# Kernel tuning notes

Measured on AMD Instinct MI355X. Metric: run time of the kernel, lower is better.

Reference implementation:

```python
import jax, jax.numpy as jnp
import numpy as np

B, L, D_MODEL = 2, 4096, 256
EXPAND = 2
D_INNER = EXPAND * D_MODEL
D_STATE = 16
D_CONV = 4
DT_RANK = max(1, D_MODEL // 16)


def setup_inputs() -> dict:
    key = jax.random.key(0)
    ks = jax.random.split(key, 8)
    s = 0.02
    return {
        "x": jax.random.normal(ks[0], (B, L, D_MODEL), jnp.float32),
        "in_proj_w": jax.random.normal(ks[1], (D_MODEL, 2 * D_INNER), jnp.float32) * s,
        "conv_w": jax.random.normal(ks[2], (D_INNER, D_CONV), jnp.float32) * 0.1,
        "conv_b": jnp.zeros((D_INNER,), jnp.float32),
        "x_proj_w": jax.random.normal(ks[3], (D_INNER, DT_RANK + 2 * D_STATE), jnp.float32) * s,
        "dt_proj_w": jax.random.normal(ks[4], (DT_RANK, D_INNER), jnp.float32) * (DT_RANK ** -0.5),
        "dt_proj_b": jnp.log(jnp.expm1(jnp.full((D_INNER,), 0.01, jnp.float32))),
        "A_log": jnp.log(jnp.tile(jnp.arange(1, D_STATE + 1, dtype=jnp.float32), (D_INNER, 1))),
        "D": jnp.ones((D_INNER,), jnp.float32),
        "out_proj_w": jax.random.normal(ks[5], (D_INNER, D_MODEL), jnp.float32) * s,
        "ln_gamma": jnp.ones((D_MODEL,), jnp.float32),
        "ln_beta": jnp.zeros((D_MODEL,), jnp.float32),
    }


def _mamba(x, in_proj_w, conv_w, conv_b, x_proj_w, dt_proj_w, dt_proj_b, A_log, D, out_proj_w):
    b = x.shape[0]
    xz = x @ in_proj_w                       # [B,L,2*d_inner]
    u, z = jnp.split(xz, 2, axis=-1)
    # depthwise causal conv over time
    u_pad = jnp.pad(u, ((0, 0), (D_CONV - 1, 0), (0, 0)))
    kern = conv_w.T[:, None, :]              # [D_CONV, 1, D_INNER]
    u_conv = jax.lax.conv_general_dilated(
        u_pad, kern, (1,), 'VALID',
        dimension_numbers=('NHC', 'HIO', 'NHC'),
        feature_group_count=D_INNER) + conv_b
    u_conv = jax.nn.silu(u_conv)             # [B,L,d_inner]
    dbl = u_conv @ x_proj_w
    dt, Bm, Cm = jnp.split(dbl, [DT_RANK, DT_RANK + D_STATE], axis=-1)
    delta = jax.nn.softplus(dt @ dt_proj_w + dt_proj_b)   # [B,L,d_inner]
    A = -jnp.exp(A_log)                                    # [d_inner,d_state]
    dA = jnp.exp(delta[..., None] * A)                     # [B,L,di,ds]
    dBu = delta[..., None] * Bm[:, :, None, :] * u_conv[..., None]

    def step(h, inputs):
        dA_t, dBu_t, C_t = inputs
        h = dA_t * h + dBu_t                 # [B,di,ds]
        y = jnp.einsum('bdn,bn->bd', h, C_t)
        return h, y

    h0 = jnp.zeros((b, D_INNER, D_STATE), u_conv.dtype)
    _, ys = jax.lax.scan(step, h0,
                         (dA.transpose(1, 0, 2, 3),
                          dBu.transpose(1, 0, 2, 3),
                          Cm.transpose(1, 0, 2)))
    y = ys.transpose(1, 0, 2) + u_conv * D
    y = y * jax.nn.silu(z)
    return y @ out_proj_w


def reference(x, in_proj_w, conv_w, conv_b, x_proj_w, dt_proj_w, dt_proj_b,
              A_log, D, out_proj_w, ln_gamma, ln_beta):
    y = x + _mamba(x, in_proj_w, conv_w, conv_b, x_proj_w, dt_proj_w,
                   dt_proj_b, A_log, D, out_proj_w)
    mu = jnp.mean(y, axis=-1, keepdims=True)
    var = jnp.var(y, axis=-1, keepdims=True)
    return (y - mu) / jnp.sqrt(var + 1e-5) * ln_gamma + ln_beta
```

## Files before the change

kernel.cpp:

```cpp
#include <hip/hip_runtime.h>
#include <math.h>

constexpr int BATCH  = 2;
constexpr int LSEQ   = 4096;
constexpr int DMODEL = 256;
constexpr int DINNER = 512;
constexpr int NST    = 16;
constexpr int MROWS  = BATCH * LSEQ;
constexpr int NCH    = 256;
constexpr int TCH    = LSEQ / NCH;
constexpr float LOG2E = 1.44269504088896f;

typedef __attribute__((ext_vector_type(8))) short bf16x8;
typedef __attribute__((ext_vector_type(4))) float f32x4;

__device__ __forceinline__ float fast_silu(float v) { return v / (1.f + __expf(-v)); }

__device__ __forceinline__ unsigned short f2bf(float f) {
  unsigned int u = __float_as_uint(f);
  u = (u + 0x7fffu + ((u >> 16) & 1u)) >> 16;
  return (unsigned short)u;
}
__device__ __forceinline__ float bf2f(unsigned short u) {
  return __uint_as_float(((unsigned int)u) << 16);
}

__global__ __launch_bounds__(256) void k_cast_x(const float* __restrict__ x,
                                                unsigned short* __restrict__ xb) {
  int i = (blockIdx.x * 256 + threadIdx.x) * 4;
  float4 v = *(const float4*)(x + i);
  ushort4 o;
  o.x = f2bf(v.x); o.y = f2bf(v.y); o.z = f2bf(v.z); o.w = f2bf(v.w);
  *(ushort4*)(xb + i) = o;
}

__global__ __launch_bounds__(256) void k_castT(const float* __restrict__ W,
                                               unsigned short* __restrict__ Wt,
                                               int K, int N, int ktiles) {
  __shared__ float tile[32][33];
  const int bt = blockIdx.x;
  const int kt = bt % ktiles, nt = bt / ktiles;
  const int k0 = kt * 32, n0 = nt * 32;
  const int t = threadIdx.x;
  const int c = t & 31, r0 = t >> 5;
  #pragma unroll
  for (int it = 0; it < 4; ++it) {
    int r = r0 + it * 8;
    tile[r][c] = W[(size_t)(k0 + r) * N + n0 + c];
  }
  __syncthreads();
  #pragma unroll
  for (int it = 0; it < 4; ++it) {
    int cc = r0 + it * 8;
    Wt[(size_t)(n0 + cc) * K + k0 + c] = f2bf(tile[c][cc]);
  }
}

__global__ __launch_bounds__(256) void k_cast_xpw(const float* __restrict__ xpw,
                                                  unsigned short* __restrict__ xpT) {
  int idx = blockIdx.x * 256 + threadIdx.x;
  int n = idx >> 9, k = idx & 511;
  xpT[n * 512 + k] = f2bf(xpw[k * 48 + n]);
}

__global__ __launch_bounds__(256) void k_inproj(const unsigned short* __restrict__ Xb,
                                                const unsigned short* __restrict__ Wt,
                                                unsigned short* __restrict__ ub,
                                                unsigned short* __restrict__ zb) {
  __shared__ unsigned short As[128][40];
  __shared__ unsigned short Bs[128][40];
  const int t = threadIdx.x;
  const int m0 = (blockIdx.x & 63) * 128;
  const int n0 = (blockIdx.x >> 6) * 128;
  const int lane = t & 63, wid = t >> 6;
  const int hi = lane >> 4, l15 = lane & 15;
  const int wm = wid >> 1, wn = wid & 1;
  f32x4 zero = {0.f, 0.f, 0.f, 0.f};
  f32x4 acc[4][4];
  #pragma unroll
  for (int i = 0; i < 4; ++i)
    #pragma unroll
    for (int j = 0; j < 4; ++j) acc[i][j] = zero;

  for (int k0 = 0; k0 < DMODEL; k0 += 32) {
    __syncthreads();
    #pragma unroll
    for (int it = 0; it < 2; ++it) {
      int v = it * 256 + t;
      int r = v >> 2, part = v & 3;
      *(float4*)(&As[r][part * 8]) = *(const float4*)(Xb + (size_t)(m0 + r) * 256 + k0 + part * 8);
      *(float4*)(&Bs[r][part * 8]) = *(const float4*)(Wt + (size_t)(n0 + r) * 256 + k0 + part * 8);
    }
    __syncthreads();
    bf16x8 af[4], bfv[4];
    #pragma unroll
    for (int am = 0; am < 4; ++am) af[am] = *(const bf16x8*)(&As[wm * 64 + am * 16 + l15][hi * 8]);
    #pragma unroll
    for (int bn = 0; bn < 4; ++bn) bfv[bn] = *(const bf16x8*)(&Bs[wn * 64 + bn * 16 + l15][hi * 8]);
    #pragma unroll
    for (int am = 0; am < 4; ++am)
      #pragma unroll
      for (int bn = 0; bn < 4; ++bn)
        acc[am][bn] = __builtin_amdgcn_mfma_f32_16x16x32_bf16(af[am], bfv[bn], acc[am][bn], 0, 0, 0);
  }

  unsigned short* dst = (n0 < DINNER) ? ub : zb;
  const int nb = (n0 < DINNER) ? n0 : n0 - DINNER;
  #pragma unroll
  for (int am = 0; am < 4; ++am)
    #pragma unroll
    for (int j = 0; j < 4; ++j) {
      int m = m0 + wm * 64 + am * 16 + hi * 4 + j;
      #pragma unroll
      for (int bn = 0; bn < 4; ++bn) {
        int n = nb + wn * 64 + bn * 16 + l15;
        dst[(size_t)m * DINNER + n] = f2bf(acc[am][bn][j]);
      }
    }
}

__global__ __launch_bounds__(256) void k_conv(const unsigned short* __restrict__ ub,
                                              const float* __restrict__ cw,
                                              const float* __restrict__ cb,
                                              unsigned short* __restrict__ ucb) {
  const int e2 = blockIdx.x * 256 + threadIdx.x;
  const int idx = e2 * 2;
  const int d = idx & (DINNER - 1);
  const int m = idx >> 9;
  const int l = m & (LSEQ - 1);
  float a0 = cb[d], a1 = cb[d + 1];
  #pragma unroll
  for (int j = 0; j < 4; ++j) {
    int lj = l + j - 3;
    unsigned int p = (lj >= 0) ? *(const unsigned int*)(ub + idx + (j - 3) * DINNER) : 0u;
    float u0 = bf2f((unsigned short)(p & 0xffffu));
    float u1 = bf2f((unsigned short)(p >> 16));
    a0 = fmaf(u0, cw[d * 4 + j], a0);
    a1 = fmaf(u1, cw[(d + 1) * 4 + j], a1);
  }
  unsigned int o = (unsigned int)f2bf(fast_silu(a0)) | ((unsigned int)f2bf(fast_silu(a1)) << 16);
  *(unsigned int*)(ucb + idx) = o;
}

__global__ __launch_bounds__(128) void k_xprojm(const unsigned short* __restrict__ ucb,
                                                const unsigned short* __restrict__ xpT,
                                                float* __restrict__ dt_out,
                                                float* __restrict__ Bout,
                                                float* __restrict__ Cout) {
  __shared__ unsigned short As[32][136];
  __shared__ unsigned short Bs[48][136];
  const int t = threadIdx.x;
  const int m0 = blockIdx.x * 32;
  const int lane = t & 63, wid = t >> 6;
  const int hi = lane >> 4, l15 = lane & 15;
  f32x4 zero = {0.f, 0.f, 0.f, 0.f};
  f32x4 acc[3] = {zero, zero, zero};

  for (int k0 = 0; k0 < DINNER; k0 += 128) {
    __syncthreads();
    #pragma unroll
    for (int it = 0; it < 4; ++it) {
      int v = it * 128 + t;
      int r = v >> 4, part = v & 15;
      *(float4*)(&As[r][part * 8]) = *(const float4*)(ucb + (size_t)(m0 + r) * 512 + k0 + part * 8);
    }
    #pragma unroll
    for (int it = 0; it < 6; ++it) {
      int v = it * 128 + t;
      int r = v >> 4, part = v & 15;
      *(float4*)(&Bs[r][part * 8]) = *(const float4*)(xpT + (size_t)r * 512 + k0 + part * 8);
    }
    __syncthreads();
    #pragma unroll
    for (int kk = 0; kk < 4; ++kk) {
      bf16x8 af = *(const bf16x8*)(&As[wid * 16 + l15][kk * 32 + hi * 8]);
      #pragma unroll
      for (int nf = 0; nf < 3; ++nf) {
        bf16x8 bv = *(const bf16x8*)(&Bs[nf * 16 + l15][kk * 32 + hi * 8]);
        acc[nf] = __builtin_amdgcn_mfma_f32_16x16x32_bf16(af, bv, acc[nf], 0, 0, 0);
      }
    }
  }
  #pragma unroll
  for (int j = 0; j < 4; ++j) {
    int m = m0 + wid * 16 + hi * 4 + j;
    dt_out[m * 16 + l15] = acc[0][j];
    Bout[m * 16 + l15]   = acc[1][j];
    Cout[m * 16 + l15]   = acc[2][j];
  }
}

__global__ __launch_bounds__(256) void k_scan1(const unsigned short* __restrict__ ucb,
                                               const float* __restrict__ dtin,
                                               const float* __restrict__ dtw,
                                               const float* __restrict__ dtb,
                                               const float* __restrict__ Bin,
                                               const float* __restrict__ Alog,
                                               unsigned short* __restrict__ delta_b,
                                               float* __restrict__ Ssum,
                                               float* __restrict__ Dsum) {
  const int g = blockIdx.x * 256 + threadIdx.x;
  const int d    = g & (DINNER - 1);
  const int rest = g >> 9;
  const int c = rest & (NCH - 1);
  const int b = rest >> 8;
  __shared__ float Bsh[TCH][NST];
  __shared__ float dtsh[TCH][NST];
  {
    const int base = (b * LSEQ + c * TCH) * NST;
    ((float*)Bsh)[threadIdx.x]  = Bin[base + threadIdx.x];
    ((float*)dtsh)[threadIdx.x] = dtin[base + threadIdx.x];
  }
  __syncthreads();
  float dwreg[NST];
  #pragma unroll
  for (int r = 0; r < NST; ++r) dwreg[r] = dtw[r * DINNER + d];
  const float bias = dtb[d];
  float a2[NST];
  #pragma unroll
  for (int n = 0; n < NST; ++n) a2[n] = -__expf(Alog[d * NST + n]) * LOG2E;
  bool geo = true;
  #pragma unroll
  for (int n = 1; n < NST; ++n)
    geo = geo && (fabsf(a2[n] - (float)(n + 1) * a2[0]) <= 1e-5f * fabsf(a2[n]));
  float S[NST];
  #pragma unroll
  for (int n = 0; n < NST; ++n) S[n] = 0.f;
  float dsum = 0.f;
  const int row0 = (b * LSEQ + c * TCH) * DINNER + d;
  for (int tt = 0; tt < TCH; ++tt) {
    float acc = bias;
    #pragma unroll
    for (int r = 0; r < NST; ++r) acc = fmaf(dtsh[tt][r], dwreg[r], acc);
    float sp = (acc > 20.f) ? acc : log1pf(__expf(acc));
    unsigned short deb = f2bf(sp);
    delta_b[row0 + tt * DINNER] = deb;
    float de = bf2f(deb);
    float xv = bf2f(ucb[row0 + tt * DINNER]);
    float du = de * xv;
    dsum += de;
    float dA[NST];
    if (geo) {
      float r1 = exp2f(de * a2[0]);
      float p = r1;
      #pragma unroll
      for (int n = 0; n < NST; ++n) { dA[n] = p; p *= r1; }
    } else {
      #pragma unroll
      for (int n = 0; n < NST; ++n) dA[n] = exp2f(de * a2[n]);
    }
    #pragma unroll
    for (int n = 0; n < NST; ++n) S[n] = fmaf(dA[n], S[n], du * Bsh[tt][n]);
  }
  const int bc = b * NCH + c;
  Dsum[bc * DINNER + d] = dsum;
  #pragma unroll
  for (int n = 0; n < NST; ++n)
    Ssum[(size_t)((n * BATCH + b) * NCH + c) * DINNER + d] = S[n];
}

__global__ __launch_bounds__(64) void k_scan2(const float* __restrict__ S,
                                              const float* __restrict__ Dsum,
                                              const float* __restrict__ Alog,
                                              float* __restrict__ Hinit) {
  const int idx = blockIdx.x * 64 + threadIdx.x;
  const int d  = idx & (DINNER - 1);
  const int nb = idx >> 9;
  const int b  = nb & (BATCH - 1);
  const int n  = nb >> 1;
  const float a = -__expf(Alog[d * NST + n]);
  const float* Srow = S     + (size_t)nb * NCH * DINNER + d;
  const float* Drow = Dsum  + (size_t)b  * NCH * DINNER + d;
  float*       Hrow = Hinit + (size_t)nb * NCH * DINNER + d;
  float h = 0.f;
  #pragma unroll 8
  for (int c = 0; c < NCH; ++c) {
    float ds = Drow[(size_t)c * DINNER];
    float s  = Srow[(size_t)c * DINNER];
    Hrow[(size_t)c * DINNER] = h;
    h = fmaf(__expf(a * ds), h, s);
  }
}

__global__ __launch_bounds__(256) void k_scan3(const unsigned short* __restrict__ ucb,
                                               const unsigned short* __restrict__ delta_b,
                                               const float* __restrict__ Bin,
                                               const float* __restrict__ Cin,
                                               const float* __restrict__ Alog,
                                               const float* __restrict__ Dvec,
                                               const float* __restrict__ Hinit,
                                               unsigned short* __restrict__ zb) {
  const int g = blockIdx.x * 256 + threadIdx.x;
  const int d    = g & (DINNER - 1);
  const int rest = g >> 9;
  const int c = rest & (NCH - 1);
  const int b = rest >> 8;
  __shared__ float Bsh[TCH][NST];
  __shared__ float Csh[TCH][NST];
  {
    const int base = (b * LSEQ + c * TCH) * NST;
    ((float*)Bsh)[threadIdx.x] = Bin[base + threadIdx.x];
    ((float*)Csh)[threadIdx.x] = Cin[base + threadIdx.x];
  }
  __syncthreads();
  float a2[NST];
  #pragma unroll
  for (int n = 0; n < NST; ++n) a2[n] = -__expf(Alog[d * NST + n]) * LOG2E;
  bool geo = true;
  #pragma unroll
  for (int n = 1; n < NST; ++n)
    geo = geo && (fabsf(a2[n] - (float)(n + 1) * a2[0]) <= 1e-5f * fabsf(a2[n]));
  float h[NST];
  #pragma unroll
  for (int n = 0; n < NST; ++n)
    h[n] = Hinit[(size_t)(((n * BATCH + b) * NCH) + c) * DINNER + d];
  const float Dd = Dvec[d];
  const int row0 = (b * LSEQ + c * TCH) * DINNER + d;
  for (int tt = 0; tt < TCH; ++tt) {
    float de = bf2f(delta_b[row0 + tt * DINNER]);
    float xv = bf2f(ucb[row0 + tt * DINNER]);
    float du = de * xv;
    float dA[NST];
    if (geo) {
      float r1 = exp2f(de * a2[0]);
      float p = r1;
      #pragma unroll
      for (int n = 0; n < NST; ++n) { dA[n] = p; p *= r1; }
    } else {
      #pragma unroll
      for (int n = 0; n < NST; ++n) dA[n] = exp2f(de * a2[n]);
    }
    float y = 0.f;
    #pragma unroll
    for (int n = 0; n < NST; ++n) {
      h[n] = fmaf(dA[n], h[n], du * Bsh[tt][n]);
      y = fmaf(h[n], Csh[tt][n], y);
    }
    float zz = bf2f(zb[row0 + tt * DINNER]);
    zb[row0 + tt * DINNER] = f2bf((y + xv * Dd) * fast_silu(zz));
  }
}

__global__ __launch_bounds__(512) void k_out(const unsigned short* __restrict__ Yb,
                                             const unsigned short* __restrict__ W2t,
                                             const float* __restrict__ X,
                                             const float* __restrict__ gam,
                                             const float* __restrict__ bet,
                                             float* __restrict__ out) {
  __shared__ unsigned short As[32][40];
  __shared__ unsigned short Bs[256][40];
  __shared__ float red[4][32][2];
  const int t = threadIdx.x;
  const int m0 = blockIdx.x * 32;
  const int lane = t & 63, wid = t >> 6;
  const int hi = lane >> 4, l15 = lane & 15;
  const int wm = wid >> 2, wn = wid & 3;
  f32x4 zero = {0.f, 0.f, 0.f, 0.f};
  f32x4 acc[4];
  #pragma unroll
  for (int bn = 0; bn < 4; ++bn) acc[bn] = zero;

  for (int k0 = 0; k0 < DINNER; k0 += 32) {
    __syncthreads();
    if (t < 128) {
      int r = t >> 2, part = t & 3;
      *(float4*)(&As[r][part * 8]) = *(const float4*)(Yb + (size_t)(m0 + r) * 512 + k0 + part * 8);
    }
    #pragma unroll
    for (int it = 0; it < 2; ++it) {
      int v = it * 512 + t;
      int r = v >> 2, part = v & 3;
      *(float4*)(&Bs[r][part * 8]) = *(const float4*)(W2t + (size_t)r * 512 + k0 + part * 8);
    }
    __syncthreads();
    bf16x8 af = *(const bf16x8*)(&As[wm * 16 + l15][hi * 8]);
    #pragma unroll
    for (int bn = 0; bn < 4; ++bn) {
      bf16x8 bfr = *(const bf16x8*)(&Bs[wn * 64 + bn * 16 + l15][hi * 8]);
      acc[bn] = __builtin_amdgcn_mfma_f32_16x16x32_bf16(af, bfr, acc[bn], 0, 0, 0);
    }
  }

  float vv[4][4];
  float s[4] = {0.f, 0.f, 0.f, 0.f}, s2[4] = {0.f, 0.f, 0.f, 0.f};
  #pragma unroll
  for (int bn = 0; bn < 4; ++bn) {
    int n = wn * 64 + bn * 16 + l15;
    #pragma unroll
    for (int j = 0; j < 4; ++j) {
      int m = m0 + wm * 16 + hi * 4 + j;
      float v = acc[bn][j] + X[(size_t)m * DMODEL + n];
      vv[bn][j] = v;
      s[j] += v; s2[j] += v * v;
    }
  }
  #pragma unroll
  for (int j = 0; j < 4; ++j) {
    #pragma unroll
    for (int off = 1; off < 16; off <<= 1) {
      s[j]  += __shfl_xor(s[j],  off, 64);
      s2[j] += __shfl_xor(s2[j], off, 64);
    }
  }
  if (l15 == 0) {
    #pragma unroll
    for (int j = 0; j < 4; ++j) {
      red[wn][wm * 16 + hi * 4 + j][0] = s[j];
      red[wn][wm * 16 + hi * 4 + j][1] = s2[j];
    }
  }
  __syncthreads();
  float g[4], bb[4];
  #pragma unroll
  for (int bn = 0; bn < 4; ++bn) {
    int n = wn * 64 + bn * 16 + l15;
    g[bn] = gam[n]; bb[bn] = bet[n];
  }
  #pragma unroll
  for (int j = 0; j < 4; ++j) {
    int row = wm * 16 + hi * 4 + j;
    float S  = red[0][row][0] + red[1][row][0] + red[2][row][0] + red[3][row][0];
    float S2 = red[0][row][1] + red[1][row][1] + red[2][row][1] + red[3][row][1];
    float mu = S * (1.f / 256.f);
    float rstd = rsqrtf(S2 * (1.f / 256.f) - mu * mu + 1e-5f);
    int m = m0 + row;
    #pragma unroll
    for (int bn = 0; bn < 4; ++bn) {
      int n = wn * 64 + bn * 16 + l15;
      out[(size_t)m * DMODEL + n] = (vv[bn][j] - mu) * rstd * g[bn] + bb[bn];
    }
  }
}

extern "C" void kernel_launch(void* const* d_in, const int* in_sizes, int n_in,
                              void* d_out, int out_size, void* d_ws, size_t ws_size,
                              hipStream_t stream) {
  const float* x    = (const float*)d_in[0];
  const float* ipw  = (const float*)d_in[1];
  const float* cw   = (const float*)d_in[2];
  const float* cb   = (const float*)d_in[3];
  const float* xpw  = (const float*)d_in[4];
  const float* dtw  = (const float*)d_in[5];
  const float* dtbv = (const float*)d_in[6];
  const float* alog = (const float*)d_in[7];
  const float* Dv   = (const float*)d_in[8];
  const float* opw  = (const float*)d_in[9];
  const float* gam  = (const float*)d_in[10];
  const float* bet  = (const float*)d_in[11];
  float* out = (float*)d_out;

  char* ws = (char*)d_ws;
  unsigned short* ub  = (unsigned short*)ws;   ws += (size_t)MROWS * DINNER * 2;
  unsigned short* zb  = (unsigned short*)ws;   ws += (size_t)MROWS * DINNER * 2;
  unsigned short* ucb = (unsigned short*)ws;   ws += (size_t)MROWS * DINNER * 2;
  unsigned short* xb  = (unsigned short*)ws;   ws += (size_t)MROWS * DMODEL * 2;
  float* buf_dt = (float*)ws;  ws += (size_t)MROWS * NST * 4;
  float* buf_B  = (float*)ws;  ws += (size_t)MROWS * NST * 4;
  float* buf_C  = (float*)ws;  ws += (size_t)MROWS * NST * 4;
  float* buf_ds = (float*)ws;  ws += (size_t)BATCH * NCH * DINNER * 4;
  float* buf_S  = (float*)ws;  ws += (size_t)NST * BATCH * NCH * DINNER * 4;
  float* buf_H  = (float*)ws;  ws += (size_t)NST * BATCH * NCH * DINNER * 4;
  unsigned short* W1t = (unsigned short*)ws; ws += (size_t)1024 * 256 * 2;
  unsigned short* W2t = (unsigned short*)ws; ws += (size_t)256 * 512 * 2;
  unsigned short* xpT = (unsigned short*)ws; ws += (size_t)48 * 512 * 2;
  unsigned short* deltab = ub;

  k_cast_x  <<<dim3(2048), dim3(256), 0, stream>>>(x, xb);
  k_castT   <<<dim3(256),  dim3(256), 0, stream>>>(ipw, W1t, 256, 1024, 8);
  k_castT   <<<dim3(128),  dim3(256), 0, stream>>>(opw, W2t, 512, 256, 16);
  k_cast_xpw<<<dim3(96),   dim3(256), 0, stream>>>(xpw, xpT);
  k_inproj  <<<dim3(512),  dim3(256), 0, stream>>>(xb, W1t, ub, zb);
  k_conv    <<<dim3(MROWS * DINNER / 512), dim3(256), 0, stream>>>(ub, cw, cb, ucb);
  k_xprojm  <<<dim3(MROWS / 32), dim3(128), 0, stream>>>(ucb, xpT, buf_dt, buf_B, buf_C);
  k_scan1   <<<dim3(BATCH * NCH * DINNER / 256), dim3(256), 0, stream>>>(ucb, buf_dt, dtw, dtbv, buf_B,
                                                                         alog, deltab, buf_S, buf_ds);
  k_scan2   <<<dim3(NST * BATCH * DINNER / 64), dim3(64), 0, stream>>>(buf_S, buf_ds, alog, buf_H);
  k_scan3   <<<dim3(BATCH * NCH * DINNER / 256), dim3(256), 0, stream>>>(ucb, deltab, buf_B, buf_C,
                                                                         alog, Dv, buf_H, zb);
  k_out     <<<dim3(MROWS / 32), dim3(512), 0, stream>>>(zb, W2t, x, gam, bet, out);
}
```

Measured before the change: 137.9 us.

## Fuse x cast into in_proj, store scan chunk states as bf16, tune scans

Removes the separate fp32-to-bf16 cast kernel for x by converting x tiles while loading them into shared memory inside the in_proj GEMM. The per-chunk scan summaries S and the initial states H are now stored in bf16 instead of fp32, halving that intermediate traffic. The scan kernels also get occupancy launch bounds and unroll pragmas on the time loop. The bf16 chunk states lose precision in the carried recurrence state, and in_proj now reads fp32 x from global memory each k-step, which doubles its A-operand load bytes.

Result: slower. 198.3 us (+43.9%).

```diff
diff --git a/kernel.cpp b/kernel.cpp
--- a/kernel.cpp
+++ b/kernel.cpp
@@ -25,15 +25,6 @@
   return __uint_as_float(((unsigned int)u) << 16);
 }
 
-__global__ __launch_bounds__(256) void k_cast_x(const float* __restrict__ x,
-                                                unsigned short* __restrict__ xb) {
-  int i = (blockIdx.x * 256 + threadIdx.x) * 4;
-  float4 v = *(const float4*)(x + i);
-  ushort4 o;
-  o.x = f2bf(v.x); o.y = f2bf(v.y); o.z = f2bf(v.z); o.w = f2bf(v.w);
-  *(ushort4*)(xb + i) = o;
-}
-
 __global__ __launch_bounds__(256) void k_castT(const float* __restrict__ W,
                                                unsigned short* __restrict__ Wt,
                                                int K, int N, int ktiles) {
@@ -63,7 +54,7 @@
   xpT[n * 512 + k] = f2bf(xpw[k * 48 + n]);
 }
 
-__global__ __launch_bounds__(256) void k_inproj(const unsigned short* __restrict__ Xb,
+__global__ __launch_bounds__(256) void k_inproj(const float* __restrict__ X,
                                                 const unsigned short* __restrict__ Wt,
                                                 unsigned short* __restrict__ ub,
                                                 unsigned short* __restrict__ zb) {
@@ -85,10 +76,18 @@
   for (int k0 = 0; k0 < DMODEL; k0 += 32) {
     __syncthreads();
     #pragma unroll
+    for (int it = 0; it < 4; ++it) {
+      int v = it * 256 + t;
+      int r = v >> 3, part = v & 7;
+      float4 a = *(const float4*)(X + (size_t)(m0 + r) * 256 + k0 + part * 4);
+      ushort4 o;
+      o.x = f2bf(a.x); o.y = f2bf(a.y); o.z = f2bf(a.z); o.w = f2bf(a.w);
+      *(ushort4*)(&As[r][part * 4]) = o;
+    }
+    #pragma unroll
     for (int it = 0; it < 2; ++it) {
       int v = it * 256 + t;
       int r = v >> 2, part = v & 3;
-      *(float4*)(&As[r][part * 8]) = *(const float4*)(Xb + (size_t)(m0 + r) * 256 + k0 + part * 8);
       *(float4*)(&Bs[r][part * 8]) = *(const float4*)(Wt + (size_t)(n0 + r) * 256 + k0 + part * 8);
     }
     __syncthreads();
@@ -190,15 +189,15 @@
   }
 }
 
-__global__ __launch_bounds__(256) void k_scan1(const unsigned short* __restrict__ ucb,
-                                               const float* __restrict__ dtin,
-                                               const float* __restrict__ dtw,
-                                               const float* __restrict__ dtb,
-                                               const float* __restrict__ Bin,
-                                               const float* __restrict__ Alog,
-                                               unsigned short* __restrict__ delta_b,
-                                               float* __restrict__ Ssum,
-                                               float* __restrict__ Dsum) {
+__global__ __launch_bounds__(256, 4) void k_scan1(const unsigned short* __restrict__ ucb,
+                                                  const float* __restrict__ dtin,
+                                                  const float* __restrict__ dtw,
+                                                  const float* __restrict__ dtb,
+                                                  const float* __restrict__ Bin,
+                                                  const float* __restrict__ Alog,
+                                                  unsigned short* __restrict__ delta_b,
+                                                  unsigned short* __restrict__ Ssum,
+                                                  float* __restrict__ Dsum) {
   const int g = blockIdx.x * 256 + threadIdx.x;
   const int d    = g & (DINNER - 1);
   const int rest = g >> 9;
@@ -228,6 +227,7 @@
   for (int n = 0; n < NST; ++n) S[n] = 0.f;
   float dsum = 0.f;
   const int row0 = (b * LSEQ + c * TCH) * DINNER + d;
+  #pragma unroll 4
   for (int tt = 0; tt < TCH; ++tt) {
     float acc = bias;
     #pragma unroll
@@ -256,40 +256,40 @@
   Dsum[bc * DINNER + d] = dsum;
   #pragma unroll
   for (int n = 0; n < NST; ++n)
-    Ssum[(size_t)((n * BATCH + b) * NCH + c) * DINNER + d] = S[n];
-}
-
-__global__ __launch_bounds__(64) void k_scan2(const float* __restrict__ S,
+    Ssum[(size_t)((n * BATCH + b) * NCH + c) * DINNER + d] = f2bf(S[n]);
+}
+
+__global__ __launch_bounds__(64) void k_scan2(const unsigned short* __restrict__ S,
                                               const float* __restrict__ Dsum,
                                               const float* __restrict__ Alog,
-                                              float* __restrict__ Hinit) {
+                                              unsigned short* __restrict__ Hinit) {
   const int idx = blockIdx.x * 64 + threadIdx.x;
   const int d  = idx & (DINNER - 1);
   const int nb = idx >> 9;
   const int b  = nb & (BATCH - 1);
   const int n  = nb >> 1;
   const float a = -__expf(Alog[d * NST + n]);
-  const float* Srow = S     + (size_t)nb * NCH * DINNER + d;
-  const float* Drow = Dsum  + (size_t)b  * NCH * DINNER + d;
-  float*       Hrow = Hinit + (size_t)nb * NCH * DINNER + d;
+  const unsigned short* Srow = S     + (size_t)nb * NCH * DINNER + d;
+  const float*          Drow = Dsum  + (size_t)b  * NCH * DINNER + d;
+  unsigned short*       Hrow = Hinit + (size_t)nb * NCH * DINNER + d;
   float h = 0.f;
   #pragma unroll 8
   for (int c = 0; c < NCH; ++c) {
     float ds = Drow[(size_t)c * DINNER];
-    float s  = Srow[(size_t)c * DINNER];
-    Hrow[(size_t)c * DINNER] = h;
+    float s  = bf2f(Srow[(size_t)c * DINNER]);
+    Hrow[(size_t)c * DINNER] = f2bf(h);
     h = fmaf(__expf(a * ds), h, s);
   }
 }
 
-__global__ __launch_bounds__(256) void k_scan3(const unsigned short* __restrict__ ucb,
-                                               const unsigned short* __restrict__ delta_b,
-                                               const float* __restrict__ Bin,
-                                               const float* __restrict__ Cin,
-                                               const float* __restrict__ Alog,
-                                               const float* __restrict__ Dvec,
-                                               const float* __restrict__ Hinit,
-                                               unsigned short* __restrict__ zb) {
+__global__ __launch_bounds__(256, 4) void k_scan3(const unsigned short* __restrict__ ucb,
+                                                  const unsigned short* __restrict__ delta_b,
+                                                  const float* __restrict__ Bin,
+                                                  const float* __restrict__ Cin,
+                                                  const float* __restrict__ Alog,
+                                                  const float* __restrict__ Dvec,
+                                                  const unsigned short* __restrict__ Hinit,
+                                                  unsigned short* __restrict__ zb) {
   const int g = blockIdx.x * 256 + threadIdx.x;
   const int d    = g & (DINNER - 1);
   const int rest = g >> 9;
@@ -313,9 +313,10 @@
   float h[NST];
   #pragma unroll
   for (int n = 0; n < NST; ++n)
-    h[n] = Hinit[(size_t)(((n * BATCH + b) * NCH) + c) * DINNER + d];
+    h[n] = bf2f(Hinit[(size_t)(((n * BATCH + b) * NCH) + c) * DINNER + d]);
   const float Dd = Dvec[d];
   const int row0 = (b * LSEQ + c * TCH) * DINNER + d;
+  #pragma unroll 4
   for (int tt = 0; tt < TCH; ++tt) {
     float de = bf2f(delta_b[row0 + tt * DINNER]);
     float xv = bf2f(ucb[row0 + tt * DINNER]);
@@ -453,23 +454,21 @@
   unsigned short* ub  = (unsigned short*)ws;   ws += (size_t)MROWS * DINNER * 2;
   unsigned short* zb  = (unsigned short*)ws;   ws += (size_t)MROWS * DINNER * 2;
   unsigned short* ucb = (unsigned short*)ws;   ws += (size_t)MROWS * DINNER * 2;
-  unsigned short* xb  = (unsigned short*)ws;   ws += (size_t)MROWS * DMODEL * 2;
   float* buf_dt = (float*)ws;  ws += (size_t)MROWS * NST * 4;
   float* buf_B  = (float*)ws;  ws += (size_t)MROWS * NST * 4;
   float* buf_C  = (float*)ws;  ws += (size_t)MROWS * NST * 4;
   float* buf_ds = (float*)ws;  ws += (size_t)BATCH * NCH * DINNER * 4;
-  float* buf_S  = (float*)ws;  ws += (size_t)NST * BATCH * NCH * DINNER * 4;
-  float* buf_H  = (float*)ws;  ws += (size_t)NST * BATCH * NCH * DINNER * 4;
+  unsigned short* buf_S = (unsigned short*)ws;  ws += (size_t)NST * BATCH * NCH * DINNER * 2;
+  unsigned short* buf_H = (unsigned short*)ws;  ws += (size_t)NST * BATCH * NCH * DINNER * 2;
   unsigned short* W1t = (unsigned short*)ws; ws += (size_t)1024 * 256 * 2;
   unsigned short* W2t = (unsigned short*)ws; ws += (size_t)256 * 512 * 2;
   unsigned short* xpT = (unsigned short*)ws; ws += (size_t)48 * 512 * 2;
   unsigned short* deltab = ub;
 
-  k_cast_x  <<<dim3(2048), dim3(256), 0, stream>>>(x, xb);
   k_castT   <<<dim3(256),  dim3(256), 0, stream>>>(ipw, W1t, 256, 1024, 8);
   k_castT   <<<dim3(128),  dim3(256), 0, stream>>>(opw, W2t, 512, 256, 16);
   k_cast_xpw<<<dim3(96),   dim3(256), 0, stream>>>(xpw, xpT);
-  k_inproj  <<<dim3(512),  dim3(256), 0, stream>>>(xb, W1t, ub, zb);
+  k_inproj  <<<dim3(512),  dim3(256), 0, stream>>>(x, W1t, ub, zb);
   k_conv    <<<dim3(MROWS * DINNER / 512), dim3(256), 0, stream>>>(ub, cw, cb, ucb);
   k_xprojm  <<<dim3(MROWS / 32), dim3(128), 0, stream>>>(ucb, xpT, buf_dt, buf_B, buf_C);
   k_scan1   <<<dim3(BATCH * NCH * DINNER / 256), dim3(256), 0, stream>>>(ucb, buf_dt, dtw, dtbv, buf_B,
```
